# Kernel optimization log

Measured on AMD Instinct MI355X. Metric: run time of the kernel, lower is better.

The kernel has to match this reference:

```python
import jax, jax.numpy as jnp
import numpy as np
from jax import lax

B, N, C = 8, 16384, 96
ROPE_BASE = 10000.0


def _rope(x):
    """Faithful port of the module's RoPE. x: (b, h, w, c).
    Note: the original computes angles over the h axis but, due to torch
    broadcasting of (h, k_max) against (b, h, w, k_max), the rotation is
    applied along the w axis (valid since h == w)."""
    b, h, w, c = x.shape
    k_max = c // 2
    theta = 1.0 / (ROPE_BASE ** (jnp.arange(k_max, dtype=x.dtype) / k_max))  # (k_max,)
    angles = jnp.arange(h, dtype=x.dtype)[:, None] * theta                  # (h, k_max)
    cos = jnp.cos(angles)[None, None, :, :]  # broadcast over w axis
    sin = jnp.sin(angles)[None, None, :, :]
    xr = x.reshape(b, h, w, k_max, 2)
    xre, xim = xr[..., 0], xr[..., 1]
    ore = xre * cos - xim * sin
    oim = xre * sin + xim * cos
    return jnp.stack([ore, oim], axis=-1).reshape(b, h, w, c)


def setup_inputs() -> dict:
    key = jax.random.key(0)
    ks = jax.random.split(key, 5)
    return {
        "x": jax.random.normal(ks[0], (B, N, C), dtype=jnp.float32),
        "qk_w": jax.random.normal(ks[1], (2 * C, C), dtype=jnp.float32) * 0.05,
        "qk_b": jax.random.normal(ks[2], (2 * C,), dtype=jnp.float32) * 0.02,
        "lepe_w": jax.random.normal(ks[3], (C, 1, 3, 3), dtype=jnp.float32) * 0.1,
        "lepe_b": jax.random.normal(ks[4], (C,), dtype=jnp.float32) * 0.02,
        "num_heads": 4,
    }


def reference(x, qk_w, qk_b, lepe_w, lepe_b, num_heads):
    b, n, c = x.shape
    h = w = int(round(n ** 0.5))
    d = c // num_heads
    inv_sqrt_n = float(n) ** (-0.5)

    qk = x @ qk_w.T + qk_b                        # (b, n, 2c)
    q = jax.nn.elu(qk[..., :c]) + 1.0             # (b, n, c)
    k = jax.nn.elu(qk[..., c:]) + 1.0
    v = x

    q_rope = _rope(q.reshape(b, h, w, c)).reshape(b, n, num_heads, d).transpose(0, 2, 1, 3)
    k_rope = _rope(k.reshape(b, h, w, c)).reshape(b, n, num_heads, d).transpose(0, 2, 1, 3)
    qh = q.reshape(b, n, num_heads, d).transpose(0, 2, 1, 3)  # (b, H, n, d)
    kh = k.reshape(b, n, num_heads, d).transpose(0, 2, 1, 3)
    vh = v.reshape(b, n, num_heads, d).transpose(0, 2, 1, 3)

    k_mean = kh.mean(axis=2, keepdims=True)                         # (b, H, 1, d)
    z = 1.0 / (jnp.einsum('bhnd,bhmd->bhnm', qh, k_mean) + 1e-6)    # (b, H, n, 1)
    kv = jnp.einsum('bhnd,bhne->bhde', k_rope * inv_sqrt_n, vh * inv_sqrt_n)  # (b, H, d, d)
    out = jnp.einsum('bhnd,bhde->bhne', q_rope, kv) * z             # (b, H, n, d)
    out = out.transpose(0, 2, 1, 3).reshape(b, n, c)

    # LePE: depthwise 3x3 conv on v laid out as (b, c, h, w)
    v_img = vh.transpose(0, 2, 1, 3).reshape(b, h, w, c).transpose(0, 3, 1, 2)
    lepe = lax.conv_general_dilated(
        v_img, lepe_w, window_strides=(1, 1), padding='SAME',
        feature_group_count=c, dimension_numbers=('NCHW', 'OIHW', 'NCHW'))
    lepe = lepe + lepe_b[None, :, None, None]
    return out + lepe.transpose(0, 2, 3, 1).reshape(b, n, c)
```

## Files before the change

kernel.cpp:

```cpp
#include <hip/hip_runtime.h>


#define NLINE 16384
#define CCH 96
#define XSP 104
#define KTP 136
#define QSP 98
#define OP2 100
#define THETA_COEF 0.2768273412406135f

typedef __attribute__((ext_vector_type(4))) float f32x4;
typedef __attribute__((ext_vector_type(8))) short bf16x8;

__device__ __forceinline__ unsigned short f2bf(float f) {
  unsigned int u = __float_as_uint(f);
  u += 0x7FFFu + ((u >> 16) & 1u);
  return (unsigned short)(u >> 16);
}
__device__ __forceinline__ float bf2f(unsigned short h) {
  return __uint_as_float(((unsigned int)h) << 16);
}
__device__ __forceinline__ void store_bf4(unsigned short* dst, f32x4 v) {
  unsigned long long pk = (unsigned long long)f2bf(v.x)
    | ((unsigned long long)f2bf(v.y) << 16)
    | ((unsigned long long)f2bf(v.z) << 32)
    | ((unsigned long long)f2bf(v.w) << 48);
  *(unsigned long long*)dst = pk;
}

__global__ void prep_w(const float* __restrict__ qkw, unsigned short* __restrict__ wfrag) {
  int u = blockIdx.x * 256 + threadIdx.x;
  if (u >= 2304) return;
  int lane = u & 63;
  int nt = (u >> 6) % 6;
  int rest = u / 384;
  int kk = rest % 3, half = rest / 3;
  int lr = lane & 15, q4 = lane >> 4;
  const float* src = qkw + (half * 96 + nt * 16 + lr) * 96 + kk * 32 + q4 * 8;
  unsigned short* dst = wfrag + (size_t)u * 8;
#pragma unroll
  for (int j = 0; j < 8; ++j) dst[j] = f2bf(src[j]);
}

__global__ __launch_bounds__(256, 3) void la_k1(
    const float* __restrict__ x, const unsigned short* __restrict__ wfrag,
    const float* __restrict__ qkb, float* __restrict__ kv_g,
    float* __restrict__ ksum_g)
{
  const int tid  = threadIdx.x;
  const int b    = blockIdx.x >> 7;
  const int tile = blockIdx.x & 127;

  __shared__ alignas(16) unsigned short xs[128 * XSP];
  __shared__ alignas(16) unsigned short kqt[96 * KTP];
  __shared__ float ksum_s[96];

  if (tid < 96) ksum_s[tid] = 0.0f;

  const int wave = tid >> 6;
  const int lane = tid & 63;
  const int lr   = lane & 15;
  const int q4   = lane >> 4;
  const int row0 = wave * 32;

  float biasv[6];
#pragma unroll
  for (int nt = 0; nt < 6; ++nt) biasv[nt] = qkb[96 + nt * 16 + lr];

  const float* xb = x + ((size_t)b * NLINE + (size_t)tile * 128) * CCH;
  for (int i = tid; i < 3072; i += 256) {
    int r = i / 24, c4 = i % 24;
    int sw = (r >> 3) & 3;
    store_bf4(&xs[r * XSP + ((((c4 >> 1) ^ sw) << 3) | ((c4 & 1) << 2))],
              ((const f32x4*)xb)[i]);
  }
  __syncthreads();

  f32x4 acc[2][6];
#pragma unroll
  for (int mt = 0; mt < 2; ++mt)
#pragma unroll
    for (int nt = 0; nt < 6; ++nt) acc[mt][nt] = (f32x4){0.f, 0.f, 0.f, 0.f};

#pragma unroll
  for (int kk = 0; kk < 3; ++kk) {
    const int g = kk * 4 + q4;
    const int r1 = row0 + lr, r2 = row0 + 16 + lr;
    bf16x8 a0 = *(const bf16x8*)&xs[r1 * XSP + ((g ^ ((r1 >> 3) & 3)) << 3)];
    bf16x8 a1 = *(const bf16x8*)&xs[r2 * XSP + ((g ^ ((r2 >> 3) & 3)) << 3)];
#pragma unroll
    for (int nt = 0; nt < 6; ++nt) {
      bf16x8 bf = *(const bf16x8*)&wfrag[(size_t)(((3 + kk) * 6 + nt) * 64 + lane) * 8];
      acc[0][nt] = __builtin_amdgcn_mfma_f32_16x16x32_bf16(a0, bf, acc[0][nt], 0, 0, 0);
      acc[1][nt] = __builtin_amdgcn_mfma_f32_16x16x32_bf16(a1, bf, acc[1][nt], 0, 0, 0);
    }
  }

#pragma unroll
  for (int nt = 0; nt < 6; ++nt) {
    const int col = nt * 16 + lr;
    const float bias = biasv[nt];
    float csum = 0.0f;
#pragma unroll
    for (int mt = 0; mt < 2; ++mt)
#pragma unroll
      for (int rg = 0; rg < 4; ++rg) {
        int row = row0 + mt * 16 + q4 * 4 + rg;
        float v = acc[mt][nt][rg] + bias;
        v = (v > 0.0f) ? (v + 1.0f) : __expf(v);
        csum += v;
        kqt[col * KTP + row] = f2bf(v);
      }
    atomicAdd(&ksum_s[col], csum);
  }
  __syncthreads();

  if (tid < 96) atomicAdd(&ksum_g[b * 96 + tid], ksum_s[tid]);

  {
    const int r = tid & 127;
    const int cp0 = tid >> 7;
    float theta = exp2f(-THETA_COEF * (float)cp0);
    const float fstep = exp2f(-2.0f * THETA_COEF);
#pragma unroll 4
    for (int s = 0; s < 24; ++s) {
      int cp = cp0 + 2 * s;
      float re = bf2f(kqt[(2 * cp) * KTP + r]);
      float im = bf2f(kqt[(2 * cp + 1) * KTP + r]);
      float sn, cn;
      __sincosf((float)r * theta, &sn, &cn);
      kqt[(2 * cp) * KTP + r]     = f2bf(re * cn - im * sn);
      kqt[(2 * cp + 1) * KTP + r] = f2bf(re * sn + im * cn);
      theta *= fstep;
    }
  }
  __syncthreads();

  const int h = wave;
  f32x4 kvacc[2][2];
#pragma unroll
  for (int mt = 0; mt < 2; ++mt)
#pragma unroll
    for (int nt = 0; nt < 2; ++nt) kvacc[mt][nt] = (f32x4){0.f, 0.f, 0.f, 0.f};

#pragma unroll
  for (int kk = 0; kk < 4; ++kk) {
    const int rbase = kk * 32 + q4 * 8;
    const int sw = (rbase >> 3) & 3;
    bf16x8 afr[2], bfr[2];
#pragma unroll
    for (int mt = 0; mt < 2; ++mt) {
      int c = 24 * h + mt * 16 + lr; if (c > 95) c = 95;
      afr[mt] = *(const bf16x8*)&kqt[c * KTP + rbase];
    }
#pragma unroll
    for (int nt = 0; nt < 2; ++nt) {
      int c = 24 * h + nt * 16 + lr; if (c > 95) c = 95;
      const int off = (((c >> 3) ^ sw) << 3) | (c & 7);
#pragma unroll
      for (int j = 0; j < 8; ++j) bfr[nt][j] = (short)xs[(rbase + j) * XSP + off];
    }
#pragma unroll
    for (int mt = 0; mt < 2; ++mt)
#pragma unroll
      for (int nt = 0; nt < 2; ++nt)
        kvacc[mt][nt] = __builtin_amdgcn_mfma_f32_16x16x32_bf16(afr[mt], bfr[nt], kvacc[mt][nt], 0, 0, 0);
  }

  const float inv_n = 1.0f / 16384.0f;
  float* kvb = kv_g + ((size_t)b * 4 + h) * 576;
#pragma unroll
  for (int mt = 0; mt < 2; ++mt)
#pragma unroll
    for (int rg = 0; rg < 4; ++rg) {
      int d = mt * 16 + q4 * 4 + rg;
      if (d < 24) {
#pragma unroll
        for (int nt = 0; nt < 2; ++nt) {
          int e = nt * 16 + lr;
          if (e < 24) atomicAdd(&kvb[d * 24 + e], kvacc[mt][nt][rg] * inv_n);
        }
      }
    }
}

__global__ __launch_bounds__(256, 5) void la_k2(
    const float* __restrict__ x, const unsigned short* __restrict__ wfrag,
    const float* __restrict__ qkb, const float* __restrict__ lepe_w,
    const float* __restrict__ lepe_b, const float* __restrict__ kv_g,
    const float* __restrict__ ksum_g, float* __restrict__ out)
{
  const int tid = threadIdx.x;
  const int b   = blockIdx.x & 7;
  const int seg = blockIdx.x >> 3;
  const int y   = seg >> 1;

  __shared__ alignas(16) unsigned short qs[64 * QSP];
  __shared__ _Float16 outs[64 * OP2];
  __shared__ float lepe_s[9 * 96];
  __shared__ float theta_s[48];

  if (tid < 48) theta_s[tid] = exp2f(-THETA_COEF * (float)tid);
  for (int i = tid; i < 864; i += 256) {
    int ch = i / 9, tap = i % 9;
    lepe_s[tap * 96 + ch] = lepe_w[i];
  }

  const int wave = tid >> 6;
  const int lane = tid & 63;
  const int lr   = lane & 15;
  const int q4   = lane >> 4;

  float biasv[6];
#pragma unroll
  for (int nt = 0; nt < 6; ++nt) biasv[nt] = qkb[nt * 16 + lr];

  const float* xb = x + ((size_t)b * NLINE + (size_t)seg * 64) * CCH;
  bf16x8 afrag[3];
#pragma unroll
  for (int kk = 0; kk < 3; ++kk) {
    const float* ap = xb + (wave * 16 + lr) * CCH + kk * 32 + q4 * 8;
    f32x4 v0 = ((const f32x4*)ap)[0];
    f32x4 v1 = ((const f32x4*)ap)[1];
    afrag[kk][0] = (short)f2bf(v0.x); afrag[kk][1] = (short)f2bf(v0.y);
    afrag[kk][2] = (short)f2bf(v0.z); afrag[kk][3] = (short)f2bf(v0.w);
    afrag[kk][4] = (short)f2bf(v1.x); afrag[kk][5] = (short)f2bf(v1.y);
    afrag[kk][6] = (short)f2bf(v1.z); afrag[kk][7] = (short)f2bf(v1.w);
  }

  f32x4 acc[6];
#pragma unroll
  for (int nt = 0; nt < 6; ++nt) acc[nt] = (f32x4){0.f, 0.f, 0.f, 0.f};
#pragma unroll
  for (int kk = 0; kk < 3; ++kk) {
#pragma unroll
    for (int nt = 0; nt < 6; ++nt) {
      bf16x8 bf = *(const bf16x8*)&wfrag[(size_t)((kk * 6 + nt) * 64 + lane) * 8];
      acc[nt] = __builtin_amdgcn_mfma_f32_16x16x32_bf16(afrag[kk], bf, acc[nt], 0, 0, 0);
    }
  }
#pragma unroll
  for (int nt = 0; nt < 6; ++nt) {
    const int col = nt * 16 + lr;
    const float bias = biasv[nt];
#pragma unroll
    for (int rg = 0; rg < 4; ++rg) {
      int t = wave * 16 + q4 * 4 + rg;
      float v = acc[nt][rg] + bias;
      v = (v > 0.0f) ? (v + 1.0f) : __expf(v);
      qs[t * QSP + col] = f2bf(v);
    }
  }
  __syncthreads();

  {
    const int t  = lane;
    const int h  = __builtin_amdgcn_readfirstlane(wave);
    const int xw = ((seg & 1) << 6) + t;
    const float inv_n = 1.0f / 16384.0f;

    float qv[24];
    const unsigned int* qrow = (const unsigned int*)&qs[t * QSP + 24 * h];
#pragma unroll
    for (int u = 0; u < 12; ++u) {
      unsigned int w = qrow[u];
      qv[2 * u]     = bf2f((unsigned short)(w & 0xFFFFu));
      qv[2 * u + 1] = bf2f((unsigned short)(w >> 16));
    }

    const float* km = ksum_g + b * 96 + 24 * h;
    float dot = 0.0f;
#pragma unroll
    for (int d2 = 0; d2 < 24; ++d2) dot += qv[d2] * km[d2];
    const float z = 1.0f / (dot * inv_n + 1e-6f);

    float qr[24];
#pragma unroll
    for (int jj = 0; jj < 12; ++jj) {
      float sn, cn;
      __sincosf((float)xw * theta_s[12 * h + jj], &sn, &cn);
      float re = qv[2 * jj], im = qv[2 * jj + 1];
      qr[2 * jj]     = re * cn - im * sn;
      qr[2 * jj + 1] = re * sn + im * cn;
    }

    const float* kvh = kv_g + ((size_t)b * 4 + h) * 576;
    float res[24];
#pragma unroll
    for (int e = 0; e < 24; ++e) res[e] = 0.0f;
    for (int d2 = 0; d2 < 24; ++d2) {
      float qd = qr[d2];
#pragma unroll
      for (int e = 0; e < 24; ++e) res[e] += qd * kvh[d2 * 24 + e];
    }
    const float* lb = lepe_b + 24 * h;
#pragma unroll
    for (int e = 0; e < 24; ++e)
      outs[t * OP2 + 24 * h + e] = (_Float16)(res[e] * z + lb[e]);
  }
  __syncthreads();

  float* ob = out + ((size_t)b * NLINE + (size_t)seg * 64) * CCH;
  const float* xg = x + (size_t)b * NLINE * CCH;
#pragma unroll
  for (int k = 0; k < 6; ++k) {
    int idx = tid + 256 * k;
    int tl = idx / 24, c4 = idx % 24;
    int ch0 = c4 * 4;
    int xw = ((seg & 1) << 6) + tl;

    float r0 = (float)outs[tl * OP2 + ch0];
    float r1 = (float)outs[tl * OP2 + ch0 + 1];
    float r2 = (float)outs[tl * OP2 + ch0 + 2];
    float r3 = (float)outs[tl * OP2 + ch0 + 3];

#pragma unroll
    for (int dy = 0; dy < 3; ++dy) {
      int yy = y + dy - 1;
      if (yy < 0 || yy > 127) continue;
      const float* rowp = xg + ((size_t)yy * 128) * CCH;
#pragma unroll
      for (int dx = 0; dx < 3; ++dx) {
        int xx = xw + dx - 1;
        if (xx < 0 || xx > 127) continue;
        f32x4 v = *(const f32x4*)(rowp + xx * CCH + ch0);
        const float* wp = &lepe_s[(dy * 3 + dx) * 96 + ch0];
        r0 += wp[0] * v.x;
        r1 += wp[1] * v.y;
        r2 += wp[2] * v.z;
        r3 += wp[3] * v.w;
      }
    }
    f32x4 o = { r0, r1, r2, r3 };
    ((f32x4*)ob)[idx] = o;
  }
}

extern "C" void kernel_launch(void* const* d_in, const int* in_sizes, int n_in,
                              void* d_out, int out_size, void* d_ws, size_t ws_size,
                              hipStream_t stream) {
  const float* x      = (const float*)d_in[0];
  const float* qkw    = (const float*)d_in[1];
  const float* qkb    = (const float*)d_in[2];
  const float* lepe_w = (const float*)d_in[3];
  const float* lepe_b = (const float*)d_in[4];
  float* out = (float*)d_out;

  unsigned short* wfrag = (unsigned short*)d_ws;
  float* kv_g   = (float*)((char*)d_ws + 36864);
  float* ksum_g = kv_g + 18432;

  hipMemsetAsync(kv_g, 0, 19200 * sizeof(float), stream);
  prep_w<<<dim3(9), dim3(256), 0, stream>>>(qkw, wfrag);
  la_k1<<<dim3(1024), dim3(256), 0, stream>>>(x, wfrag, qkb, kv_g, ksum_g);
  la_k2<<<dim3(2048), dim3(256), 0, stream>>>(x, wfrag, qkb, lepe_w, lepe_b, kv_g, ksum_g, out);
}
```

Measured before the change: 184.0 us.

## Drop x LDS staging in k1, fuse RoPE into epilogue, shrink LDS in k2

la_k1 no longer stages x in shared memory. A fragments are loaded directly from global memory into registers, and V fragments are gathered from global memory and converted to bf16. RoPE for k is folded into the GEMM epilogue using a lane shuffle and the hardware sin/cos instructions on revolutions, which removes a separate LDS pass and a barrier. la_k2 reuses the qs buffer for packed fp16 output, computes theta inline, and raises the occupancy hints. The strided scalar global gathers for V and the lower-precision hardware sin on large angles add memory traffic and accuracy risk.

```diff
diff --git a/kernel.cpp b/kernel.cpp
--- a/kernel.cpp
+++ b/kernel.cpp
@@ -3,14 +3,14 @@
 
 #define NLINE 16384
 #define CCH 96
-#define XSP 104
 #define KTP 136
 #define QSP 98
-#define OP2 100
 #define THETA_COEF 0.2768273412406135f
+#define LOG2_2PI   2.6514961294723187f
 
 typedef __attribute__((ext_vector_type(4))) float f32x4;
 typedef __attribute__((ext_vector_type(8))) short bf16x8;
+typedef __attribute__((ext_vector_type(2))) __fp16 fp16x2;
 
 __device__ __forceinline__ unsigned short f2bf(float f) {
   unsigned int u = __float_as_uint(f);
@@ -20,12 +20,13 @@
 __device__ __forceinline__ float bf2f(unsigned short h) {
   return __uint_as_float(((unsigned int)h) << 16);
 }
-__device__ __forceinline__ void store_bf4(unsigned short* dst, f32x4 v) {
-  unsigned long long pk = (unsigned long long)f2bf(v.x)
-    | ((unsigned long long)f2bf(v.y) << 16)
-    | ((unsigned long long)f2bf(v.z) << 32)
-    | ((unsigned long long)f2bf(v.w) << 48);
-  *(unsigned long long*)dst = pk;
+__device__ __forceinline__ bf16x8 pack_bf8(f32x4 v0, f32x4 v1) {
+  bf16x8 r;
+  r[0] = (short)f2bf(v0.x); r[1] = (short)f2bf(v0.y);
+  r[2] = (short)f2bf(v0.z); r[3] = (short)f2bf(v0.w);
+  r[4] = (short)f2bf(v1.x); r[5] = (short)f2bf(v1.y);
+  r[6] = (short)f2bf(v1.z); r[7] = (short)f2bf(v1.w);
+  return r;
 }
 
 __global__ void prep_w(const float* __restrict__ qkw, unsigned short* __restrict__ wfrag) {
@@ -42,7 +43,7 @@
   for (int j = 0; j < 8; ++j) dst[j] = f2bf(src[j]);
 }
 
-__global__ __launch_bounds__(256, 3) void la_k1(
+__global__ __launch_bounds__(256, 4) void la_k1(
     const float* __restrict__ x, const unsigned short* __restrict__ wfrag,
     const float* __restrict__ qkb, float* __restrict__ kv_g,
     float* __restrict__ ksum_g)
@@ -51,31 +52,32 @@
   const int b    = blockIdx.x >> 7;
   const int tile = blockIdx.x & 127;
 
-  __shared__ alignas(16) unsigned short xs[128 * XSP];
   __shared__ alignas(16) unsigned short kqt[96 * KTP];
   __shared__ float ksum_s[96];
 
   if (tid < 96) ksum_s[tid] = 0.0f;
+  __syncthreads();
 
   const int wave = tid >> 6;
   const int lane = tid & 63;
   const int lr   = lane & 15;
   const int q4   = lane >> 4;
   const int row0 = wave * 32;
+  const float* xb = x + ((size_t)b * NLINE + (size_t)tile * 128) * CCH;
+
+  bf16x8 afr[2][3];
+#pragma unroll
+  for (int mt = 0; mt < 2; ++mt)
+#pragma unroll
+    for (int kk = 0; kk < 3; ++kk) {
+      const float* ap = xb + (row0 + mt * 16 + lr) * CCH + kk * 32 + q4 * 8;
+      afr[mt][kk] = pack_bf8(((const f32x4*)ap)[0], ((const f32x4*)ap)[1]);
+    }
 
   float biasv[6];
 #pragma unroll
   for (int nt = 0; nt < 6; ++nt) biasv[nt] = qkb[96 + nt * 16 + lr];
 
-  const float* xb = x + ((size_t)b * NLINE + (size_t)tile * 128) * CCH;
-  for (int i = tid; i < 3072; i += 256) {
-    int r = i / 24, c4 = i % 24;
-    int sw = (r >> 3) & 3;
-    store_bf4(&xs[r * XSP + ((((c4 >> 1) ^ sw) << 3) | ((c4 & 1) << 2))],
-              ((const f32x4*)xb)[i]);
-  }
-  __syncthreads();
-
   f32x4 acc[2][6];
 #pragma unroll
   for (int mt = 0; mt < 2; ++mt)
@@ -84,57 +86,51 @@
 
 #pragma unroll
   for (int kk = 0; kk < 3; ++kk) {
-    const int g = kk * 4 + q4;
-    const int r1 = row0 + lr, r2 = row0 + 16 + lr;
-    bf16x8 a0 = *(const bf16x8*)&xs[r1 * XSP + ((g ^ ((r1 >> 3) & 3)) << 3)];
-    bf16x8 a1 = *(const bf16x8*)&xs[r2 * XSP + ((g ^ ((r2 >> 3) & 3)) << 3)];
 #pragma unroll
     for (int nt = 0; nt < 6; ++nt) {
       bf16x8 bf = *(const bf16x8*)&wfrag[(size_t)(((3 + kk) * 6 + nt) * 64 + lane) * 8];
-      acc[0][nt] = __builtin_amdgcn_mfma_f32_16x16x32_bf16(a0, bf, acc[0][nt], 0, 0, 0);
-      acc[1][nt] = __builtin_amdgcn_mfma_f32_16x16x32_bf16(a1, bf, acc[1][nt], 0, 0, 0);
-    }
-  }
-
+      acc[0][nt] = __builtin_amdgcn_mfma_f32_16x16x32_bf16(afr[0][kk], bf, acc[0][nt], 0, 0, 0);
+      acc[1][nt] = __builtin_amdgcn_mfma_f32_16x16x32_bf16(afr[1][kk], bf, acc[1][nt], 0, 0, 0);
+    }
+  }
+
+  const int odd = lr & 1;
 #pragma unroll
   for (int nt = 0; nt < 6; ++nt) {
     const int col = nt * 16 + lr;
-    const float bias = biasv[nt];
+    const float threv = exp2f(-THETA_COEF * (float)(col >> 1) - LOG2_2PI);
     float csum = 0.0f;
+    float vv[2][4];
 #pragma unroll
     for (int mt = 0; mt < 2; ++mt)
 #pragma unroll
       for (int rg = 0; rg < 4; ++rg) {
-        int row = row0 + mt * 16 + q4 * 4 + rg;
-        float v = acc[mt][nt][rg] + bias;
+        float v = acc[mt][nt][rg] + biasv[nt];
         v = (v > 0.0f) ? (v + 1.0f) : __expf(v);
         csum += v;
-        kqt[col * KTP + row] = f2bf(v);
+        vv[mt][rg] = v;
       }
     atomicAdd(&ksum_s[col], csum);
+#pragma unroll
+    for (int mt = 0; mt < 2; ++mt) {
+      unsigned long long pk = 0;
+#pragma unroll
+      for (int rg = 0; rg < 4; ++rg) {
+        float p = __shfl_xor(vv[mt][rg], 1);
+        int r = row0 + mt * 16 + q4 * 4 + rg;
+        float rev = (float)r * threv;
+        float sn = __builtin_amdgcn_sinf(rev);
+        float cn = __builtin_amdgcn_cosf(rev);
+        float o = odd ? (p * sn + vv[mt][rg] * cn)
+                      : (vv[mt][rg] * cn - p * sn);
+        pk |= (unsigned long long)f2bf(o) << (16 * rg);
+      }
+      *(unsigned long long*)&kqt[col * KTP + row0 + mt * 16 + q4 * 4] = pk;
+    }
   }
   __syncthreads();
 
   if (tid < 96) atomicAdd(&ksum_g[b * 96 + tid], ksum_s[tid]);
-
-  {
-    const int r = tid & 127;
-    const int cp0 = tid >> 7;
-    float theta = exp2f(-THETA_COEF * (float)cp0);
-    const float fstep = exp2f(-2.0f * THETA_COEF);
-#pragma unroll 4
-    for (int s = 0; s < 24; ++s) {
-      int cp = cp0 + 2 * s;
-      float re = bf2f(kqt[(2 * cp) * KTP + r]);
-      float im = bf2f(kqt[(2 * cp + 1) * KTP + r]);
-      float sn, cn;
-      __sincosf((float)r * theta, &sn, &cn);
-      kqt[(2 * cp) * KTP + r]     = f2bf(re * cn - im * sn);
-      kqt[(2 * cp + 1) * KTP + r] = f2bf(re * sn + im * cn);
-      theta *= fstep;
-    }
-  }
-  __syncthreads();
 
   const int h = wave;
   f32x4 kvacc[2][2];
@@ -146,25 +142,24 @@
 #pragma unroll
   for (int kk = 0; kk < 4; ++kk) {
     const int rbase = kk * 32 + q4 * 8;
-    const int sw = (rbase >> 3) & 3;
-    bf16x8 afr[2], bfr[2];
+    bf16x8 ka[2], vb[2];
 #pragma unroll
     for (int mt = 0; mt < 2; ++mt) {
       int c = 24 * h + mt * 16 + lr; if (c > 95) c = 95;
-      afr[mt] = *(const bf16x8*)&kqt[c * KTP + rbase];
+      ka[mt] = *(const bf16x8*)&kqt[c * KTP + rbase];
     }
 #pragma unroll
     for (int nt = 0; nt < 2; ++nt) {
       int c = 24 * h + nt * 16 + lr; if (c > 95) c = 95;
-      const int off = (((c >> 3) ^ sw) << 3) | (c & 7);
-#pragma unroll
-      for (int j = 0; j < 8; ++j) bfr[nt][j] = (short)xs[(rbase + j) * XSP + off];
+#pragma unroll
+      for (int j = 0; j < 8; ++j)
+        vb[nt][j] = (short)f2bf(xb[(rbase + j) * CCH + c]);
     }
 #pragma unroll
     for (int mt = 0; mt < 2; ++mt)
 #pragma unroll
       for (int nt = 0; nt < 2; ++nt)
-        kvacc[mt][nt] = __builtin_amdgcn_mfma_f32_16x16x32_bf16(afr[mt], bfr[nt], kvacc[mt][nt], 0, 0, 0);
+        kvacc[mt][nt] = __builtin_amdgcn_mfma_f32_16x16x32_bf16(ka[mt], vb[nt], kvacc[mt][nt], 0, 0, 0);
   }
 
   const float inv_n = 1.0f / 16384.0f;
@@ -184,7 +179,7 @@
     }
 }
 
-__global__ __launch_bounds__(256, 5) void la_k2(
+__global__ __launch_bounds__(256, 8) void la_k2(
     const float* __restrict__ x, const unsigned short* __restrict__ wfrag,
     const float* __restrict__ qkb, const float* __restrict__ lepe_w,
     const float* __restrict__ lepe_b, const float* __restrict__ kv_g,
@@ -196,11 +191,8 @@
   const int y   = seg >> 1;
 
   __shared__ alignas(16) unsigned short qs[64 * QSP];
-  __shared__ _Float16 outs[64 * OP2];
   __shared__ float lepe_s[9 * 96];
-  __shared__ float theta_s[48];
-
-  if (tid < 48) theta_s[tid] = exp2f(-THETA_COEF * (float)tid);
+
   for (int i = tid; i < 864; i += 256) {
     int ch = i / 9, tap = i % 9;
     lepe_s[tap * 96 + ch] = lepe_w[i];
@@ -220,12 +212,7 @@
 #pragma unroll
   for (int kk = 0; kk < 3; ++kk) {
     const float* ap = xb + (wave * 16 + lr) * CCH + kk * 32 + q4 * 8;
-    f32x4 v0 = ((const f32x4*)ap)[0];
-    f32x4 v1 = ((const f32x4*)ap)[1];
-    afrag[kk][0] = (short)f2bf(v0.x); afrag[kk][1] = (short)f2bf(v0.y);
-    afrag[kk][2] = (short)f2bf(v0.z); afrag[kk][3] = (short)f2bf(v0.w);
-    afrag[kk][4] = (short)f2bf(v1.x); afrag[kk][5] = (short)f2bf(v1.y);
-    afrag[kk][6] = (short)f2bf(v1.z); afrag[kk][7] = (short)f2bf(v1.w);
+    afrag[kk] = pack_bf8(((const f32x4*)ap)[0], ((const f32x4*)ap)[1]);
   }
 
   f32x4 acc[6];
@@ -242,17 +229,17 @@
 #pragma unroll
   for (int nt = 0; nt < 6; ++nt) {
     const int col = nt * 16 + lr;
-    const float bias = biasv[nt];
 #pragma unroll
     for (int rg = 0; rg < 4; ++rg) {
       int t = wave * 16 + q4 * 4 + rg;
-      float v = acc[nt][rg] + bias;
+      float v = acc[nt][rg] + biasv[nt];
       v = (v > 0.0f) ? (v + 1.0f) : __expf(v);
       qs[t * QSP + col] = f2bf(v);
     }
   }
   __syncthreads();
 
+  float res[24];
   {
     const int t  = lane;
     const int h  = __builtin_amdgcn_readfirstlane(wave);
@@ -274,29 +261,40 @@
     for (int d2 = 0; d2 < 24; ++d2) dot += qv[d2] * km[d2];
     const float z = 1.0f / (dot * inv_n + 1e-6f);
 
-    float qr[24];
 #pragma unroll
     for (int jj = 0; jj < 12; ++jj) {
-      float sn, cn;
-      __sincosf((float)xw * theta_s[12 * h + jj], &sn, &cn);
+      float threv = exp2f(-THETA_COEF * (float)(12 * h + jj) - LOG2_2PI);
+      float rev = (float)xw * threv;
+      float sn = __builtin_amdgcn_sinf(rev);
+      float cn = __builtin_amdgcn_cosf(rev);
       float re = qv[2 * jj], im = qv[2 * jj + 1];
-      qr[2 * jj]     = re * cn - im * sn;
-      qr[2 * jj + 1] = re * sn + im * cn;
+      qv[2 * jj]     = re * cn - im * sn;
+      qv[2 * jj + 1] = re * sn + im * cn;
     }
 
     const float* kvh = kv_g + ((size_t)b * 4 + h) * 576;
-    float res[24];
 #pragma unroll
     for (int e = 0; e < 24; ++e) res[e] = 0.0f;
     for (int d2 = 0; d2 < 24; ++d2) {
-      float qd = qr[d2];
+      float qd = qv[d2];
 #pragma unroll
       for (int e = 0; e < 24; ++e) res[e] += qd * kvh[d2 * 24 + e];
     }
     const float* lb = lepe_b + 24 * h;
 #pragma unroll
-    for (int e = 0; e < 24; ++e)
-      outs[t * OP2 + 24 * h + e] = (_Float16)(res[e] * z + lb[e]);
+    for (int e = 0; e < 24; ++e) res[e] = res[e] * z + lb[e];
+  }
+  __syncthreads();
+
+  __fp16* outs = (__fp16*)qs;
+  {
+    const int t = lane;
+    const int h = wave;
+#pragma unroll
+    for (int u = 0; u < 12; ++u) {
+      fp16x2 pk = __builtin_amdgcn_cvt_pkrtz(res[2 * u], res[2 * u + 1]);
+      *(fp16x2*)&outs[t * 96 + 24 * h + 2 * u] = pk;
+    }
   }
   __syncthreads();
 
@@ -309,10 +307,10 @@
     int ch0 = c4 * 4;
     int xw = ((seg & 1) << 6) + tl;
 
-    float r0 = (float)outs[tl * OP2 + ch0];
-    float r1 = (float)outs[tl * OP2 + ch0 + 1];
-    float r2 = (float)outs[tl * OP2 + ch0 + 2];
-    float r3 = (float)outs[tl * OP2 + ch0 + 3];
+    fp16x2 p0 = *(const fp16x2*)&outs[tl * 96 + ch0];
+    fp16x2 p1 = *(const fp16x2*)&outs[tl * 96 + ch0 + 2];
+    float r0 = (float)p0[0], r1 = (float)p0[1];
+    float r2 = (float)p1[0], r3 = (float)p1[1];
 
 #pragma unroll
     for (int dy = 0; dy < 3; ++dy) {
@@ -350,7 +348,7 @@
   float* kv_g   = (float*)((char*)d_ws + 36864);
   float* ksum_g = kv_g + 18432;
 
-  hipMemsetAsync(kv_g, 0, 19200 * sizeof(float), stream);
+  (void)hipMemsetAsync(kv_g, 0, 19200 * sizeof(float), stream);
   prep_w<<<dim3(9), dim3(256), 0, stream>>>(qkw, wfrag);
   la_k1<<<dim3(1024), dim3(256), 0, stream>>>(x, wfrag, qkb, kv_g, ksum_g);
   la_k2<<<dim3(2048), dim3(256), 0, stream>>>(x, wfrag, qkb, lepe_w, lepe_b, kv_g, ksum_g, out);
```

Result: faster. 175.8 us (-4.5%).
